# Kernel tuning notes

Measured on AMD Instinct MI355X. Metric: run time of the kernel, lower is better.

Reference implementation:

```python
import jax, jax.numpy as jnp
import numpy as np
import math

LOG_2PI = math.log(2.0 * math.pi)

def mv_gaussian_log_prob(value, mu, sig_diags, event_shape):
    # sig_diags acts as per-dim std (matches torch source: diff**2 / sig**2)
    diff = value - mu
    M = jnp.sum((diff / sig_diags) ** 2, axis=-1)
    half_log_det = jnp.sum(jnp.log(sig_diags), axis=-1)
    return -0.5 * (event_shape * LOG_2PI + M) - half_log_det

def setup_inputs() -> dict:
    key = jax.random.key(0)
    ks = jax.random.split(key, 18)
    N, Yd, Xd, K, S = 8192, 512, 64, 16, 10
    d = {}
    d['Y'] = jax.random.normal(ks[0], (N, Yd), jnp.float32)
    d['We_mu'] = jax.random.normal(ks[1], (Yd, Xd), jnp.float32) * 0.05
    d['be_mu'] = jnp.zeros((Xd,), jnp.float32)
    d['We_sig'] = jax.random.normal(ks[2], (Yd, Xd), jnp.float32) * 0.05
    d['be_sig'] = jnp.zeros((Xd,), jnp.float32)
    d['Wd_mu'] = jax.random.normal(ks[3], (Xd, Yd), jnp.float32) * 0.05
    d['bd_mu'] = jnp.zeros((Yd,), jnp.float32)
    d['Wd_sig'] = jax.random.normal(ks[4], (Xd, Yd), jnp.float32) * 0.05
    d['bd_sig'] = jnp.zeros((Yd,), jnp.float32)
    d['phi_mus'] = jax.random.normal(ks[5], (K, Xd), jnp.float32)
    d['phi_sigs'] = jax.random.uniform(ks[6], (K, Xd), jnp.float32, 0.5, 1.5)
    d['phi_logits'] = jax.random.normal(ks[7], (K,), jnp.float32)
    d['theta_mus'] = jax.random.normal(ks[8], (K, Xd), jnp.float32)
    d['theta_sigs'] = jax.random.uniform(ks[9], (K, Xd), jnp.float32, 0.5, 1.5)
    d['theta_logits'] = jax.random.normal(ks[10], (K,), jnp.float32)
    d['u_noise'] = jax.random.uniform(ks[11], (N, S, K), jnp.float32, 1e-6, 1.0 - 1e-6)
    d['eps_noise'] = jax.random.normal(ks[12], (N * S, Xd), jnp.float32)
    d['temperature'] = jnp.ones((1,), jnp.float32)
    return d

def reference(Y, We_mu, be_mu, We_sig, be_sig, Wd_mu, bd_mu, Wd_sig, bd_sig,
              phi_mus, phi_sigs, phi_logits, theta_mus, theta_sigs, theta_logits,
              u_noise, eps_noise, temperature):
    N, Yd = Y.shape
    K, Xd = phi_mus.shape
    S = u_noise.shape[1]
    # encoder: diagonal Gaussian q(x|y)
    enc_mu = Y @ We_mu + be_mu                                   # [N,Xd]
    enc_sig = jax.nn.softplus(Y @ We_sig + be_sig) + 1e-3        # [N,Xd]
    # cluster responsibilities (vectorized over k)
    log_pi = jax.nn.log_softmax(phi_logits)                      # [K]
    std_k = enc_sig[:, None, :] + phi_sigs[None, :, :]           # [N,K,Xd]
    z_logits = log_pi[None, :] + mv_gaussian_log_prob(
        enc_mu[:, None, :], phi_mus[None, :, :], std_k, Xd)      # [N,K]
    z_log_probs = jax.nn.log_softmax(z_logits, axis=-1)
    # per-cluster posterior (diagonal precision-weighted combination)
    inv_enc = 1.0 / enc_sig                                      # [N,Xd]
    inv_gmm = 1.0 / phi_sigs                                     # [K,Xd]
    Sig_t = 1.0 / (inv_enc[:, None, :] + inv_gmm[None, :, :])    # [N,K,Xd]
    mu_t = Sig_t * ((inv_enc * enc_mu)[:, None, :] + (inv_gmm * phi_mus)[None, :, :])
    # relaxed one-hot (gumbel-softmax) samples, probs = exp(z_log_probs)
    g = -jnp.log(-jnp.log(u_noise))                              # [N,S,K]
    z = jax.nn.softmax((z_log_probs[:, None, :] + g) / temperature[0], axis=-1)
    mu_s = jnp.einsum('bsk,bkd->bsd', z, mu_t).reshape(N * S, Xd)
    Sig_s = jnp.einsum('bsk,bkd->bsd', z, Sig_t).reshape(N * S, Xd)
    th_mu = jnp.einsum('bsk,kd->bsd', z, theta_mus).reshape(N * S, Xd)
    th_sig = jnp.einsum('bsk,kd->bsd', z, theta_sigs).reshape(N * S, Xd)
    ph_mu = jnp.einsum('bsk,kd->bsd', z, phi_mus).reshape(N * S, Xd)
    ph_sig = jnp.einsum('bsk,kd->bsd', z, phi_sigs).reshape(N * S, Xd)
    # reparameterized latent samples (diag cov -> std = sqrt)
    x_samp = mu_s + jnp.sqrt(Sig_s) * eps_noise                  # [N*S,Xd]
    # decoder
    mu_y = x_samp @ Wd_mu + bd_mu
    sig_y = jax.nn.softplus(x_samp @ Wd_sig + bd_sig) + 1e-3
    Yr = jnp.broadcast_to(Y[:, None, :], (N, S, Yd)).reshape(N * S, Yd)
    enc_mu_r = jnp.broadcast_to(enc_mu[:, None, :], (N, S, Xd)).reshape(N * S, Xd)
    enc_sig_r = jnp.broadcast_to(enc_sig[:, None, :], (N, S, Xd)).reshape(N * S, Xd)
    zf = z.reshape(N * S, K)
    loss1 = mv_gaussian_log_prob(Yr, mu_y, sig_y, Yd)
    loss2 = -mv_gaussian_log_prob(x_samp, enc_mu_r, enc_sig_r, Xd)
    loss3 = (mv_gaussian_log_prob(x_samp, th_mu, th_sig, Xd)
             + jnp.sum(jax.nn.log_softmax(theta_logits) * zf, axis=1))
    loss4 = -(mv_gaussian_log_prob(x_samp, ph_mu, ph_sig, Xd)
              + jnp.sum((z_log_probs[:, None, :] * z).reshape(N * S, K), axis=1))
    loss5 = jnp.sum(jnp.log(jnp.sum(jnp.exp(z_log_probs), axis=1)))
    return -(jnp.sum(loss1 + loss2 + loss3 + loss4) / S + loss5)
```

## Files before the change

kernel.cpp:

```cpp
#include <hip/hip_runtime.h>
#include <math.h>

#define YD 512
#define XD 64
#define KK 16
#define SS 10

typedef __attribute__((ext_vector_type(8))) short short8;
typedef __attribute__((ext_vector_type(4))) float f32x4;

__device__ __forceinline__ float wave_sum(float v) {
#pragma unroll
    for (int off = 32; off > 0; off >>= 1) v += __shfl_xor(v, off, 64);
    return v;
}

__device__ __forceinline__ float fast_rcp(float x) {
    return __builtin_amdgcn_rcpf(x);
}

__device__ __forceinline__ float bcast(float v, int l) {
    return __uint_as_float((unsigned int)__builtin_amdgcn_readlane((int)__float_as_uint(v), l));
}

__device__ __forceinline__ float softplusf(float x) {
    return fmaxf(x, 0.0f) + __logf(1.0f + __expf(-fabsf(x)));
}

__device__ __forceinline__ unsigned short f32_to_bf16(float f) {
    union { float f; unsigned int u; } v; v.f = f;
    unsigned int r = v.u + 0x7fffu + ((v.u >> 16) & 1u);
    return (unsigned short)(r >> 16);
}

__device__ __forceinline__ unsigned int pack2_bf16(float a, float b) {
    unsigned int ua = __float_as_uint(a), ub = __float_as_uint(b);
    ua = (ua + 0x7fffu + ((ua >> 16) & 1u)) >> 16;
    ub = (ub + 0x7fffu + ((ub >> 16) & 1u)) & 0xffff0000u;
    return ua | ub;
}

__global__ __launch_bounds__(256) void prep_kernel(
    const float* __restrict__ Wd_mu, const float* __restrict__ Wd_sig,
    const float* __restrict__ We_mu, const float* __restrict__ We_sig,
    const float* __restrict__ phi_mus, const float* __restrict__ phi_sigs,
    const float* __restrict__ theta_mus, const float* __restrict__ theta_sigs,
    const float* __restrict__ theta_logits,
    unsigned short* __restrict__ wmu_s, unsigned short* __restrict__ wsg_s,
    unsigned short* __restrict__ wenc,
    float4* __restrict__ tab4, float* __restrict__ lsetp)
{
    int idx = blockIdx.x * 256 + threadIdx.x;
    if (idx < 65536) {
        int mat = idx >> 15;
        int e = idx & 32767;
        int j = e & 7;
        int n = (e >> 3) & 15;
        int q = (e >> 7) & 7;
        int tg = e >> 10;
        int k = q * 8 + j;
        int col = tg * 16 + n;
        const float* W = mat ? Wd_sig : Wd_mu;
        unsigned short* o = mat ? wsg_s : wmu_s;
        o[e] = f32_to_bf16(W[k * YD + col]);
    } else if (idx < 131072) {
        int ii = idx - 65536;
        int mat = ii >> 15;
        int e = ii & 32767;
        int j = e & 7;
        int n = (e >> 3) & 15;
        int q = (e >> 7) & 3;
        int ct = (e >> 9) & 3;
        int kt = e >> 11;
        int k = kt * 32 + q * 8 + j;
        int col = ct * 16 + n;
        const float* W = mat ? We_sig : We_mu;
        wenc[mat * 32768 + e] = f32_to_bf16(W[k * XD + col]);
    } else if (idx < 131072 + 1024) {
        int e = idx - 131072;
        float4 t;
        t.x = phi_mus[e];
        t.y = phi_sigs[e];
        t.z = theta_mus[e];
        t.w = theta_sigs[e];
        tab4[e] = t;
    } else if (idx == 131072 + 1024) {
        float mt = theta_logits[0];
        for (int k = 1; k < KK; ++k) mt = fmaxf(mt, theta_logits[k]);
        float st = 0.f;
        for (int k = 0; k < KK; ++k) st += __expf(theta_logits[k] - mt);
        lsetp[0] = mt + __logf(st);
    }
}

__global__ __launch_bounds__(256) void encoder_mfma(
    const float* __restrict__ Y,
    const unsigned short* __restrict__ wenc,
    const float* __restrict__ be_mu, const float* __restrict__ be_sig,
    float* __restrict__ enc_mu, float* __restrict__ enc_sig)
{
    const int t = threadIdx.x;
    const int w = t >> 6, lane = t & 63, l16 = lane & 15, quad = lane >> 4;
    const int mat = blockIdx.x & 1;
    const int rt = blockIdx.x >> 1;
    const int row = rt * 16 + l16;
    const int ct = w;
    const unsigned short* Ws = wenc + mat * 32768;
    const float4* Yrow = (const float4*)(Y + (size_t)row * YD);

    const float* bias = mat ? be_sig : be_mu;
    float* outp = mat ? enc_sig : enc_mu;
    const int col = ct * 16 + l16;
    const float bv = bias[col];
    f32x4 acc = (f32x4){bv, bv, bv, bv};

#pragma unroll
    for (int kt = 0; kt < 16; ++kt) {
        float4 y0 = Yrow[kt * 8 + quad * 2];
        float4 y1 = Yrow[kt * 8 + quad * 2 + 1];
        union { short8 s; unsigned int u[4]; } a;
        a.u[0] = pack2_bf16(y0.x, y0.y);
        a.u[1] = pack2_bf16(y0.z, y0.w);
        a.u[2] = pack2_bf16(y1.x, y1.y);
        a.u[3] = pack2_bf16(y1.z, y1.w);
        short8 b = *(const short8*)(Ws + (((kt * 4 + ct) * 4 + quad) * 16 + l16) * 8);
        acc = __builtin_amdgcn_mfma_f32_16x16x32_bf16(a.s, b, acc, 0, 0, 0);
    }

    const int base_row = rt * 16 + quad * 4;
#pragma unroll
    for (int r = 0; r < 4; ++r) {
        float v = acc[r];
        if (mat) v = softplusf(v) + 1e-3f;
        outp[(size_t)(base_row + r) * XD + col] = v;
    }
}

__global__ __launch_bounds__(256) void resp_kernel(
    const float* __restrict__ enc_mu_g, const float* __restrict__ enc_sig_g,
    const float* __restrict__ phi_mus, const float* __restrict__ phi_sigs,
    const float* __restrict__ phi_logits,
    float* __restrict__ zlp, double* __restrict__ slotsL5)
{
    __shared__ float red[4];
    const int wv = threadIdx.x >> 6;
    const int n = blockIdx.x * 4 + wv;
    const int lane = threadIdx.x & 63;
    const int kk = lane & 15;
    const int g = lane >> 4;

    const float4* em4 = (const float4*)(enc_mu_g + (size_t)n * XD + g * 16);
    const float4* es4 = (const float4*)(enc_sig_g + (size_t)n * XD + g * 16);
    const float4* pm4 = (const float4*)(phi_mus + kk * XD + g * 16);
    const float4* ps4 = (const float4*)(phi_sigs + kk * XD + g * 16);

    float part = 0.f;
#pragma unroll
    for (int q = 0; q < 4; ++q) {
        float4 em = em4[q], es = es4[q], pm = pm4[q], ps = ps4[q];
        {
            float sd = es.x + ps.x; float df = (em.x - pm.x) * fast_rcp(sd);
            part += fmaf(-0.5f * df, df, -__logf(sd));
        }
        {
            float sd = es.y + ps.y; float df = (em.y - pm.y) * fast_rcp(sd);
            part += fmaf(-0.5f * df, df, -__logf(sd));
        }
        {
            float sd = es.z + ps.z; float df = (em.z - pm.z) * fast_rcp(sd);
            part += fmaf(-0.5f * df, df, -__logf(sd));
        }
        {
            float sd = es.w + ps.w; float df = (em.w - pm.w) * fast_rcp(sd);
            part += fmaf(-0.5f * df, df, -__logf(sd));
        }
    }
    part += __shfl_xor(part, 16, 64);
    part += __shfl_xor(part, 32, 64);
    float zl = part + phi_logits[kk];

    float m = zl;
#pragma unroll
    for (int off = 1; off <= 8; off <<= 1) m = fmaxf(m, __shfl_xor(m, off, 64));
    float e = __expf(zl - m);
    float s = e;
#pragma unroll
    for (int off = 1; off <= 8; off <<= 1) s += __shfl_xor(s, off, 64);
    zl -= m + __logf(s);

    float m3 = zl;
#pragma unroll
    for (int off = 1; off <= 8; off <<= 1) m3 = fmaxf(m3, __shfl_xor(m3, off, 64));
    float e3 = __expf(zl - m3);
    float s3 = e3;
#pragma unroll
    for (int off = 1; off <= 8; off <<= 1) s3 += __shfl_xor(s3, off, 64);
    float l5 = m3 + __logf(s3);

    if (lane < KK) zlp[(size_t)n * KK + lane] = zl;

    if (lane == 0) red[wv] = l5;
    __syncthreads();
    if (threadIdx.x == 0) {
        float tt = red[0] + red[1] + red[2] + red[3];
        atomicAdd(slotsL5 + (blockIdx.x & 63), (double)tt);
    }
}

__global__ __launch_bounds__(256, 3) void sample_kernel(
    const float* __restrict__ enc_mu_g, const float* __restrict__ enc_sig_g,
    const float* __restrict__ zlp, const float4* __restrict__ tab4,
    const float* __restrict__ theta_logits, const float* __restrict__ lsetp,
    const float* __restrict__ u_noise, const float* __restrict__ eps_noise,
    const float* __restrict__ temperature,
    unsigned short* __restrict__ x_bf16, double* __restrict__ slots234)
{
    __shared__ float red[4];
    const int wv = threadIdx.x >> 6;
    const int n = blockIdx.x * 4 + wv;
    const int d = threadIdx.x & 63;
    const int kd = d & 15;

    const float invT = fast_rcp(temperature[0]);
    const float zl_l = zlp[(size_t)n * KK + kd];
    const float tl_l = theta_logits[kd];
    const float lset = lsetp[0];

    const float em = enc_mu_g[(size_t)n * XD + d];
    const float es = enc_sig_g[(size_t)n * XD + d];
    const float inv_es = fast_rcp(es);
    const float log_es = __logf(es);
    const float em_ie = inv_es * em;

    float mu[KK], Sg[KK], tm[KK], ts[KK], pm[KK], ps[KK];
#pragma unroll
    for (int k = 0; k < KK; ++k) {
        float4 tb = tab4[k * XD + d];
        pm[k] = tb.x; ps[k] = tb.y; tm[k] = tb.z; ts[k] = tb.w;
        float ig = fast_rcp(tb.y);
        Sg[k] = fast_rcp(inv_es + ig);
        mu[k] = Sg[k] * fmaf(ig, tb.x, em_ie);
    }

    float eP[3], dzP[3], dthP[3];
#pragma unroll
    for (int p = 0; p < 3; ++p) {
        int sp = p * 4 + (d >> 4);
        int spc = sp < SS ? sp : 0;
        float u = u_noise[((size_t)n * SS + spc) * KK + kd];
        float lg = (zl_l - __logf(-__logf(u))) * invT;
        float mg = lg;
        mg = fmaxf(mg, __shfl_xor(mg, 1, 64));
        mg = fmaxf(mg, __shfl_xor(mg, 2, 64));
        mg = fmaxf(mg, __shfl_xor(mg, 4, 64));
        mg = fmaxf(mg, __shfl_xor(mg, 8, 64));
        float e = __expf(lg - mg);
        float zs = e;
        zs += __shfl_xor(zs, 1, 64);
        zs += __shfl_xor(zs, 2, 64);
        zs += __shfl_xor(zs, 4, 64);
        zs += __shfl_xor(zs, 8, 64);
        e *= fast_rcp(zs);
        float pz = e * zl_l, pt = e * tl_l;
#pragma unroll
        for (int off = 1; off <= 8; off <<= 1) {
            pz += __shfl_xor(pz, off, 64);
            pt += __shfl_xor(pt, off, 64);
        }
        eP[p] = e; dzP[p] = pz; dthP[p] = pt;
    }

    float r_acc = 0.f, sc_acc = 0.f;
    const float* erow = eps_noise + (size_t)n * SS * XD + d;
    unsigned short* xrow = x_bf16 + (size_t)n * SS * XD + d;

#pragma unroll
    for (int s = 0; s < SS; ++s) {
        const int p = s >> 2, L = (s & 3) * 16;
        float ms = 0.f, Ssum = 0.f, tmu = 0.f, tsig = 0.f, pmu = 0.f, psig = 0.f;
#pragma unroll
        for (int k = 0; k < KK; ++k) {
            float ek = bcast(eP[p], L + k);
            ms   = fmaf(ek, mu[k], ms);
            Ssum = fmaf(ek, Sg[k], Ssum);
            tmu  = fmaf(ek, tm[k], tmu);
            tsig = fmaf(ek, ts[k], tsig);
            pmu  = fmaf(ek, pm[k], pmu);
            psig = fmaf(ek, ps[k], psig);
        }
        float ep = erow[s * XD];
        float x = fmaf(__builtin_amdgcn_sqrtf(Ssum), ep, ms);
        xrow[s * XD] = f32_to_bf16(x);

        float de  = (x - em) * inv_es;
        float rts = fast_rcp(tsig);
        float dt2 = (x - tmu) * rts;
        float dp  = (x - pmu) * fast_rcp(psig);
        r_acc += 0.5f * (de * de - dt2 * dt2 + dp * dp) + __logf(psig * rts);
        sc_acc += bcast(dthP[p], L) - bcast(dzP[p], L);
    }

    r_acc = fmaf((float)SS, log_es, r_acc);
    r_acc = wave_sum(r_acc);

    const float C234 = 0.5f * XD * 1.8378770664093453f;
    float total = r_acc + sc_acc + (float)SS * (C234 - lset);

    if (d == 0) red[wv] = total;
    __syncthreads();
    if (threadIdx.x == 0) {
        float t = red[0] + red[1] + red[2] + red[3];
        atomicAdd(slots234 + (blockIdx.x & 63), (double)t);
    }
}

__global__ __launch_bounds__(256) void decoder_mfma(
    const unsigned short* __restrict__ xb,
    const unsigned short* __restrict__ wmu_s,
    const unsigned short* __restrict__ wsg_s,
    const float* __restrict__ bd_mu, const float* __restrict__ bd_sig,
    const float* __restrict__ Y, double* __restrict__ slots1,
    unsigned int magicS)
{
    __shared__ float red[4];
    const int t = threadIdx.x;
    const int w = t >> 6;
    const int lane = t & 63;
    const int l16 = lane & 15;
    const int quad = lane >> 4;
    const int mb = blockIdx.x >> 3;
    const int nb = blockIdx.x & 7;

    const int mrow = mb * 64 + w * 16 + l16;
    const short8 a0 = *(const short8*)(xb + (size_t)mrow * XD + quad * 8);
    const short8 a1 = *(const short8*)(xb + (size_t)mrow * XD + 32 + quad * 8);

    f32x4 accmu[4], accsg[4];
#pragma unroll
    for (int tt = 0; tt < 4; ++tt) {
        int col = (nb * 4 + tt) * 16 + l16;
        float bm = bd_mu[col], bs = bd_sig[col];
        accmu[tt] = (f32x4){bm, bm, bm, bm};
        accsg[tt] = (f32x4){bs, bs, bs, bs};
    }

#pragma unroll
    for (int tt = 0; tt < 4; ++tt) {
        int tg = nb * 4 + tt;
        int boff = ((tg * 8 + quad) * 16 + l16) * 8;
        short8 b0 = *(const short8*)(wmu_s + boff);
        short8 b1 = *(const short8*)(wmu_s + boff + 512);
        short8 c0 = *(const short8*)(wsg_s + boff);
        short8 c1 = *(const short8*)(wsg_s + boff + 512);
        accmu[tt] = __builtin_amdgcn_mfma_f32_16x16x32_bf16(a0, b0, accmu[tt], 0, 0, 0);
        accmu[tt] = __builtin_amdgcn_mfma_f32_16x16x32_bf16(a1, b1, accmu[tt], 0, 0, 0);
        accsg[tt] = __builtin_amdgcn_mfma_f32_16x16x32_bf16(a0, c0, accsg[tt], 0, 0, 0);
        accsg[tt] = __builtin_amdgcn_mfma_f32_16x16x32_bf16(a1, c1, accsg[tt], 0, 0, 0);
    }

    float part = 0.f;
    const int m_base = mb * 64 + w * 16 + quad * 4;
#pragma unroll
    for (int r = 0; r < 4; ++r) {
        int row = m_base + r;
        unsigned int ny = (unsigned int)(((unsigned long long)(unsigned int)row * magicS) >> 35);
        const float* Yr = Y + (size_t)ny * YD + l16;
#pragma unroll
        for (int tt = 0; tt < 4; ++tt) {
            float Yv = Yr[(nb * 4 + tt) * 16];
            float sig = softplusf(accsg[tt][r]) + 1e-3f;
            float diff = (Yv - accmu[tt][r]) * fast_rcp(sig);
            part = fmaf(-0.5f * diff, diff, part) - __logf(sig);
        }
    }
    part = wave_sum(part);
    if (lane == 0) red[w] = part;
    __syncthreads();
    if (t == 0) {
        atomicAdd(slots1 + (blockIdx.x & 63),
                  (double)(red[0] + red[1] + red[2] + red[3]));
    }
}

__global__ void finalize_kernel(const double* __restrict__ slots,
                                float* __restrict__ out, int NS, int S)
{
    double l234 = 0.0, l5 = 0.0, l1 = 0.0;
    for (int i = 0; i < 64; ++i) {
        l234 += slots[i];
        l5   += slots[64 + i];
        l1   += slots[128 + i];
    }
    l1 += (double)NS * (-0.5 * (double)YD * 1.8378770664093453);
    out[0] = (float)(-((l1 + l234) / (double)S + l5));
}

extern "C" void kernel_launch(void* const* d_in, const int* in_sizes, int n_in,
                              void* d_out, int out_size, void* d_ws, size_t ws_size,
                              hipStream_t stream) {
    const float* Y            = (const float*)d_in[0];
    const float* We_mu        = (const float*)d_in[1];
    const float* be_mu        = (const float*)d_in[2];
    const float* We_sig       = (const float*)d_in[3];
    const float* be_sig       = (const float*)d_in[4];
    const float* Wd_mu        = (const float*)d_in[5];
    const float* bd_mu        = (const float*)d_in[6];
    const float* Wd_sig       = (const float*)d_in[7];
    const float* bd_sig       = (const float*)d_in[8];
    const float* phi_mus      = (const float*)d_in[9];
    const float* phi_sigs     = (const float*)d_in[10];
    const float* phi_logits   = (const float*)d_in[11];
    const float* theta_mus    = (const float*)d_in[12];
    const float* theta_sigs   = (const float*)d_in[13];
    const float* theta_logits = (const float*)d_in[14];
    const float* u_noise      = (const float*)d_in[15];
    const float* eps_noise    = (const float*)d_in[16];
    const float* temperature  = (const float*)d_in[17];

    const int N = in_sizes[0] / YD;
    const int S = in_sizes[15] / (N * KK);
    const int NS = N * S;
    const unsigned int magicS =
        (unsigned int)((((unsigned long long)1 << 35) + S - 1) / (unsigned long long)S);

    char* base = (char*)d_ws;
    double* slots = (double*)base;
    float* enc_mu  = (float*)(base + 2048);
    float* enc_sig = enc_mu + (size_t)N * XD;
    float* zlp     = enc_sig + (size_t)N * XD;
    float4* tab4   = (float4*)(zlp + (size_t)N * KK);
    float* lsetp   = (float*)(tab4 + 1024);
    unsigned short* xb    = (unsigned short*)(lsetp + 16);
    unsigned short* wmu_s = xb + (size_t)NS * XD;
    unsigned short* wsg_s = wmu_s + 32768;
    unsigned short* wenc  = wsg_s + 32768;

    hipMemsetAsync(slots, 0, 2048, stream);

    prep_kernel<<<517, 256, 0, stream>>>(Wd_mu, Wd_sig, We_mu, We_sig,
                                         phi_mus, phi_sigs, theta_mus,
                                         theta_sigs, theta_logits,
                                         wmu_s, wsg_s, wenc, tab4, lsetp);
    encoder_mfma<<<(N / 16) * 2, 256, 0, stream>>>(Y, wenc, be_mu, be_sig,
                                                   enc_mu, enc_sig);
    resp_kernel<<<N / 4, 256, 0, stream>>>(enc_mu, enc_sig, phi_mus, phi_sigs,
                                           phi_logits, zlp, slots + 64);
    sample_kernel<<<N / 4, 256, 0, stream>>>(enc_mu, enc_sig, zlp, tab4,
                                             theta_logits, lsetp,
                                             u_noise, eps_noise, temperature,
                                             xb, slots);
    decoder_mfma<<<(NS / 64) * (YD / 64), 256, 0, stream>>>(
        xb, wmu_s, wsg_s, bd_mu, bd_sig, Y, slots + 128, magicS);
    finalize_kernel<<<1, 1, 0, stream>>>(slots, (float*)d_out, NS, S);
}
```

Baseline: 220.3 us.

## Fuse responsibility into sample kernel and retile decoder to 128-row blocks

The responsibility computation (cluster log-probs and the log-sum-exp term) is merged into the sampling kernel, so zlp is no longer written and re-read through global memory and one launch goes away. The decoder now uses a 2D grid where each wave handles two 16-row groups, which reuses the weight fragments across twice as many rows. The per-element log of sigma is replaced by a log of the product of four sigmas. This adds register pressure in both kernels, and the log-of-product can lose precision or overflow if sigmas are extreme.

```diff
diff --git a/kernel.cpp b/kernel.cpp
--- a/kernel.cpp
+++ b/kernel.cpp
@@ -136,93 +136,72 @@
     }
 }
 
-__global__ __launch_bounds__(256) void resp_kernel(
+__global__ __launch_bounds__(256, 3) void fused_sample_kernel(
     const float* __restrict__ enc_mu_g, const float* __restrict__ enc_sig_g,
     const float* __restrict__ phi_mus, const float* __restrict__ phi_sigs,
-    const float* __restrict__ phi_logits,
-    float* __restrict__ zlp, double* __restrict__ slotsL5)
-{
-    __shared__ float red[4];
-    const int wv = threadIdx.x >> 6;
-    const int n = blockIdx.x * 4 + wv;
-    const int lane = threadIdx.x & 63;
-    const int kk = lane & 15;
-    const int g = lane >> 4;
-
-    const float4* em4 = (const float4*)(enc_mu_g + (size_t)n * XD + g * 16);
-    const float4* es4 = (const float4*)(enc_sig_g + (size_t)n * XD + g * 16);
-    const float4* pm4 = (const float4*)(phi_mus + kk * XD + g * 16);
-    const float4* ps4 = (const float4*)(phi_sigs + kk * XD + g * 16);
-
-    float part = 0.f;
-#pragma unroll
-    for (int q = 0; q < 4; ++q) {
-        float4 em = em4[q], es = es4[q], pm = pm4[q], ps = ps4[q];
-        {
-            float sd = es.x + ps.x; float df = (em.x - pm.x) * fast_rcp(sd);
-            part += fmaf(-0.5f * df, df, -__logf(sd));
-        }
-        {
-            float sd = es.y + ps.y; float df = (em.y - pm.y) * fast_rcp(sd);
-            part += fmaf(-0.5f * df, df, -__logf(sd));
-        }
-        {
-            float sd = es.z + ps.z; float df = (em.z - pm.z) * fast_rcp(sd);
-            part += fmaf(-0.5f * df, df, -__logf(sd));
-        }
-        {
-            float sd = es.w + ps.w; float df = (em.w - pm.w) * fast_rcp(sd);
-            part += fmaf(-0.5f * df, df, -__logf(sd));
-        }
-    }
-    part += __shfl_xor(part, 16, 64);
-    part += __shfl_xor(part, 32, 64);
-    float zl = part + phi_logits[kk];
-
-    float m = zl;
-#pragma unroll
-    for (int off = 1; off <= 8; off <<= 1) m = fmaxf(m, __shfl_xor(m, off, 64));
-    float e = __expf(zl - m);
-    float s = e;
-#pragma unroll
-    for (int off = 1; off <= 8; off <<= 1) s += __shfl_xor(s, off, 64);
-    zl -= m + __logf(s);
-
-    float m3 = zl;
-#pragma unroll
-    for (int off = 1; off <= 8; off <<= 1) m3 = fmaxf(m3, __shfl_xor(m3, off, 64));
-    float e3 = __expf(zl - m3);
-    float s3 = e3;
-#pragma unroll
-    for (int off = 1; off <= 8; off <<= 1) s3 += __shfl_xor(s3, off, 64);
-    float l5 = m3 + __logf(s3);
-
-    if (lane < KK) zlp[(size_t)n * KK + lane] = zl;
-
-    if (lane == 0) red[wv] = l5;
-    __syncthreads();
-    if (threadIdx.x == 0) {
-        float tt = red[0] + red[1] + red[2] + red[3];
-        atomicAdd(slotsL5 + (blockIdx.x & 63), (double)tt);
-    }
-}
-
-__global__ __launch_bounds__(256, 3) void sample_kernel(
-    const float* __restrict__ enc_mu_g, const float* __restrict__ enc_sig_g,
-    const float* __restrict__ zlp, const float4* __restrict__ tab4,
+    const float* __restrict__ phi_logits, const float4* __restrict__ tab4,
     const float* __restrict__ theta_logits, const float* __restrict__ lsetp,
     const float* __restrict__ u_noise, const float* __restrict__ eps_noise,
     const float* __restrict__ temperature,
-    unsigned short* __restrict__ x_bf16, double* __restrict__ slots234)
+    unsigned short* __restrict__ x_bf16, double* __restrict__ slots)
 {
-    __shared__ float red[4];
+    __shared__ float red234[4], red5[4];
     const int wv = threadIdx.x >> 6;
     const int n = blockIdx.x * 4 + wv;
     const int d = threadIdx.x & 63;
     const int kd = d & 15;
+    const int g = d >> 4;
+
+    const float4* em4 = (const float4*)(enc_mu_g + (size_t)n * XD + g * 16);
+    const float4* es4 = (const float4*)(enc_sig_g + (size_t)n * XD + g * 16);
+    const float4* pm4 = (const float4*)(phi_mus + kd * XD + g * 16);
+    const float4* ps4 = (const float4*)(phi_sigs + kd * XD + g * 16);
+
+    float part = 0.f;
+#pragma unroll
+    for (int q = 0; q < 4; ++q) {
+        float4 emv = em4[q], esv = es4[q], pmv = pm4[q], psv = ps4[q];
+        {
+            float sd = esv.x + psv.x; float df = (emv.x - pmv.x) * fast_rcp(sd);
+            part += fmaf(-0.5f * df, df, -__logf(sd));
+        }
+        {
+            float sd = esv.y + psv.y; float df = (emv.y - pmv.y) * fast_rcp(sd);
+            part += fmaf(-0.5f * df, df, -__logf(sd));
+        }
+        {
+            float sd = esv.z + psv.z; float df = (emv.z - pmv.z) * fast_rcp(sd);
+            part += fmaf(-0.5f * df, df, -__logf(sd));
+        }
+        {
+            float sd = esv.w + psv.w; float df = (emv.w - pmv.w) * fast_rcp(sd);
+            part += fmaf(-0.5f * df, df, -__logf(sd));
+        }
+    }
+    part += __shfl_xor(part, 16, 64);
+    part += __shfl_xor(part, 32, 64);
+    float zl = part + phi_logits[kd];
+
+    float m = zl;
+#pragma unroll
+    for (int off = 1; off <= 8; off <<= 1) m = fmaxf(m, __shfl_xor(m, off, 64));
+    float e0 = __expf(zl - m);
+    float s0 = e0;
+#pragma unroll
+    for (int off = 1; off <= 8; off <<= 1) s0 += __shfl_xor(s0, off, 64);
+    zl -= m + __logf(s0);
+
+    float m3 = zl;
+#pragma unroll
+    for (int off = 1; off <= 8; off <<= 1) m3 = fmaxf(m3, __shfl_xor(m3, off, 64));
+    float e3 = __expf(zl - m3);
+    float s3 = e3;
+#pragma unroll
+    for (int off = 1; off <= 8; off <<= 1) s3 += __shfl_xor(s3, off, 64);
+    float l5 = m3 + __logf(s3);
 
     const float invT = fast_rcp(temperature[0]);
-    const float zl_l = zlp[(size_t)n * KK + kd];
+    const float zl_l = zl;
     const float tl_l = theta_logits[kd];
     const float lset = lsetp[0];
 
@@ -245,7 +224,7 @@
     float eP[3], dzP[3], dthP[3];
 #pragma unroll
     for (int p = 0; p < 3; ++p) {
-        int sp = p * 4 + (d >> 4);
+        int sp = p * 4 + g;
         int spc = sp < SS ? sp : 0;
         float u = u_noise[((size_t)n * SS + spc) * KK + kd];
         float lg = (zl_l - __logf(-__logf(u))) * invT;
@@ -306,11 +285,13 @@
     const float C234 = 0.5f * XD * 1.8378770664093453f;
     float total = r_acc + sc_acc + (float)SS * (C234 - lset);
 
-    if (d == 0) red[wv] = total;
+    if (d == 0) { red234[wv] = total; red5[wv] = l5; }
     __syncthreads();
     if (threadIdx.x == 0) {
-        float t = red[0] + red[1] + red[2] + red[3];
-        atomicAdd(slots234 + (blockIdx.x & 63), (double)t);
+        atomicAdd(slots + (blockIdx.x & 63),
+                  (double)(red234[0] + red234[1] + red234[2] + red234[3]));
+        atomicAdd(slots + 64 + (blockIdx.x & 63),
+                  (double)(red5[0] + red5[1] + red5[2] + red5[3]));
     }
 }
 
@@ -328,20 +309,29 @@
     const int lane = t & 63;
     const int l16 = lane & 15;
     const int quad = lane >> 4;
-    const int mb = blockIdx.x >> 3;
-    const int nb = blockIdx.x & 7;
-
-    const int mrow = mb * 64 + w * 16 + l16;
-    const short8 a0 = *(const short8*)(xb + (size_t)mrow * XD + quad * 8);
-    const short8 a1 = *(const short8*)(xb + (size_t)mrow * XD + 32 + quad * 8);
-
-    f32x4 accmu[4], accsg[4];
+    const int mb = blockIdx.x;
+    const int nb = blockIdx.y;
+
+    const int row0 = mb * 128 + w * 32;
+
+    short8 a[2][2];
+#pragma unroll
+    for (int rg = 0; rg < 2; ++rg) {
+        const unsigned short* xp = xb + (size_t)(row0 + rg * 16 + l16) * XD + quad * 8;
+        a[rg][0] = *(const short8*)xp;
+        a[rg][1] = *(const short8*)(xp + 32);
+    }
+
+    f32x4 accmu[2][4], accsg[2][4];
 #pragma unroll
     for (int tt = 0; tt < 4; ++tt) {
-        int col = (nb * 4 + tt) * 16 + l16;
+        int col = nb * 64 + tt * 16 + l16;
         float bm = bd_mu[col], bs = bd_sig[col];
-        accmu[tt] = (f32x4){bm, bm, bm, bm};
-        accsg[tt] = (f32x4){bs, bs, bs, bs};
+#pragma unroll
+        for (int rg = 0; rg < 2; ++rg) {
+            accmu[rg][tt] = (f32x4){bm, bm, bm, bm};
+            accsg[rg][tt] = (f32x4){bs, bs, bs, bs};
+        }
     }
 
 #pragma unroll
@@ -352,32 +342,41 @@
         short8 b1 = *(const short8*)(wmu_s + boff + 512);
         short8 c0 = *(const short8*)(wsg_s + boff);
         short8 c1 = *(const short8*)(wsg_s + boff + 512);
-        accmu[tt] = __builtin_amdgcn_mfma_f32_16x16x32_bf16(a0, b0, accmu[tt], 0, 0, 0);
-        accmu[tt] = __builtin_amdgcn_mfma_f32_16x16x32_bf16(a1, b1, accmu[tt], 0, 0, 0);
-        accsg[tt] = __builtin_amdgcn_mfma_f32_16x16x32_bf16(a0, c0, accsg[tt], 0, 0, 0);
-        accsg[tt] = __builtin_amdgcn_mfma_f32_16x16x32_bf16(a1, c1, accsg[tt], 0, 0, 0);
+#pragma unroll
+        for (int rg = 0; rg < 2; ++rg) {
+            accmu[rg][tt] = __builtin_amdgcn_mfma_f32_16x16x32_bf16(a[rg][0], b0, accmu[rg][tt], 0, 0, 0);
+            accmu[rg][tt] = __builtin_amdgcn_mfma_f32_16x16x32_bf16(a[rg][1], b1, accmu[rg][tt], 0, 0, 0);
+            accsg[rg][tt] = __builtin_amdgcn_mfma_f32_16x16x32_bf16(a[rg][0], c0, accsg[rg][tt], 0, 0, 0);
+            accsg[rg][tt] = __builtin_amdgcn_mfma_f32_16x16x32_bf16(a[rg][1], c1, accsg[rg][tt], 0, 0, 0);
+        }
     }
 
     float part = 0.f;
-    const int m_base = mb * 64 + w * 16 + quad * 4;
-#pragma unroll
-    for (int r = 0; r < 4; ++r) {
-        int row = m_base + r;
-        unsigned int ny = (unsigned int)(((unsigned long long)(unsigned int)row * magicS) >> 35);
-        const float* Yr = Y + (size_t)ny * YD + l16;
-#pragma unroll
-        for (int tt = 0; tt < 4; ++tt) {
-            float Yv = Yr[(nb * 4 + tt) * 16];
-            float sig = softplusf(accsg[tt][r]) + 1e-3f;
-            float diff = (Yv - accmu[tt][r]) * fast_rcp(sig);
-            part = fmaf(-0.5f * diff, diff, part) - __logf(sig);
+#pragma unroll
+    for (int rg = 0; rg < 2; ++rg) {
+        const int m_base = row0 + rg * 16 + quad * 4;
+#pragma unroll
+        for (int r = 0; r < 4; ++r) {
+            int row = m_base + r;
+            unsigned int ny = (unsigned int)(((unsigned long long)(unsigned int)row * magicS) >> 35);
+            const float* Yr = Y + (size_t)ny * YD + nb * 64 + l16;
+            float prod = 1.0f;
+#pragma unroll
+            for (int tt = 0; tt < 4; ++tt) {
+                float Yv = Yr[tt * 16];
+                float sig = softplusf(accsg[rg][tt][r]) + 1e-3f;
+                float diff = (Yv - accmu[rg][tt][r]) * fast_rcp(sig);
+                part = fmaf(-0.5f * diff, diff, part);
+                prod *= sig;
+            }
+            part -= __logf(prod);
         }
     }
     part = wave_sum(part);
     if (lane == 0) red[w] = part;
     __syncthreads();
     if (t == 0) {
-        atomicAdd(slots1 + (blockIdx.x & 63),
+        atomicAdd(slots1 + ((blockIdx.y * gridDim.x + blockIdx.x) & 63),
                   (double)(red[0] + red[1] + red[2] + red[3]));
     }
 }
@@ -443,13 +442,12 @@
                                          wmu_s, wsg_s, wenc, tab4, lsetp);
     encoder_mfma<<<(N / 16) * 2, 256, 0, stream>>>(Y, wenc, be_mu, be_sig,
                                                    enc_mu, enc_sig);
-    resp_kernel<<<N / 4, 256, 0, stream>>>(enc_mu, enc_sig, phi_mus, phi_sigs,
-                                           phi_logits, zlp, slots + 64);
-    sample_kernel<<<N / 4, 256, 0, stream>>>(enc_mu, enc_sig, zlp, tab4,
-                                             theta_logits, lsetp,
-                                             u_noise, eps_noise, temperature,
-                                             xb, slots);
-    decoder_mfma<<<(NS / 64) * (YD / 64), 256, 0, stream>>>(
+    fused_sample_kernel<<<N / 4, 256, 0, stream>>>(enc_mu, enc_sig,
+                                                   phi_mus, phi_sigs, phi_logits,
+                                                   tab4, theta_logits, lsetp,
+                                                   u_noise, eps_noise, temperature,
+                                                   xb, slots);
+    decoder_mfma<<<dim3(NS / 128, YD / 64), 256, 0, stream>>>(
         xb, wmu_s, wsg_s, bd_mu, bd_sig, Y, slots + 128, magicS);
     finalize_kernel<<<1, 1, 0, stream>>>(slots, (float*)d_out, NS, S);
 }
```

Result: faster. 209.0 us (-5.2%).
